# Performance work log

Measured on AMD Instinct MI355X. Metric: run time of the kernel, lower is better.

## Reference

```python
import jax, jax.numpy as jnp
import numpy as np

B, S, H = 2, 4096, 256
NH, NKV = 8, 4
HD = H // NH          # 32
GROUPS = NH // NKV    # 2
ROPE_BASE = 10000.0


def _rope_cos_sin(seq_len, dim, dtype):
    inv_freq = 1.0 / (ROPE_BASE ** (jnp.arange(0, dim, 2, dtype=jnp.float32) / dim))
    t = jnp.arange(seq_len, dtype=jnp.float32)
    freqs = jnp.outer(t, inv_freq)            # [S, dim/2]
    emb = jnp.concatenate([freqs, freqs], -1)  # [S, dim]
    return jnp.cos(emb).astype(dtype), jnp.sin(emb).astype(dtype)


def _rotate_half(x):
    x1, x2 = jnp.split(x, 2, axis=-1)
    return jnp.concatenate([-x2, x1], axis=-1)


def setup_inputs() -> dict:
    key = jax.random.key(0)
    k0, k1, k2, k3, k4 = jax.random.split(key, 5)
    return {
        "hidden_states": jax.random.normal(k0, (B, S, H), jnp.float32),
        "Wq": jax.random.normal(k1, (H, H), jnp.float32) * 0.02,
        "Wk": jax.random.normal(k2, (NKV * HD, H), jnp.float32) * 0.02,
        "Wv": jax.random.normal(k3, (NKV * HD, H), jnp.float32) * 0.02,
        "Wo": jax.random.normal(k4, (H, H), jnp.float32) * 0.02,
    }


def reference(hidden_states, Wq, Wk, Wv, Wo):
    b, s, _ = hidden_states.shape
    # projections (nn.Linear: x @ W.T)
    q = (hidden_states @ Wq.T).reshape(b, s, NH, HD).transpose(0, 2, 1, 3)   # [b,nh,s,hd]
    k = (hidden_states @ Wk.T).reshape(b, s, NKV, HD).transpose(0, 2, 1, 3)  # [b,nkv,s,hd]
    v = (hidden_states @ Wv.T).reshape(b, s, NKV, HD).transpose(0, 2, 1, 3)
    # RoPE
    cos, sin = _rope_cos_sin(s, HD, hidden_states.dtype)  # [s,hd]
    q = q * cos + _rotate_half(q) * sin
    k = k * cos + _rotate_half(k) * sin
    # GQA: repeat kv heads (repeat_interleave over head dim)
    k = jnp.repeat(k, GROUPS, axis=1)  # [b,nh,s,hd]
    v = jnp.repeat(v, GROUPS, axis=1)
    # scores + causal mask
    scores = jnp.einsum('bhqd,bhkd->bhqk', q, k) / jnp.sqrt(jnp.float32(HD)).astype(q.dtype)
    causal = jnp.triu(jnp.full((s, s), -jnp.inf, dtype=scores.dtype), k=1)
    scores = scores + causal
    attn = jax.nn.softmax(scores.astype(jnp.float32), axis=-1).astype(q.dtype)
    out = jnp.einsum('bhqk,bhkd->bhqd', attn, v)          # [b,nh,s,hd]
    out = out.transpose(0, 2, 1, 3).reshape(b, s, NH * HD)
    return out @ Wo.T
```

## Files before the change

kernel.cpp:

```cpp
#include <hip/hip_runtime.h>
#include <hip/hip_bf16.h>
#include <stdint.h>

#define NB 2
#define SEQ 4096
#define HID 256
#define NHEAD 8
#define NKVH 4
#define HDIM 32

typedef __bf16 bf16;
typedef __bf16 bf16x8 __attribute__((ext_vector_type(8)));
typedef float f32x4 __attribute__((ext_vector_type(4)));

static __device__ __forceinline__ uint16_t bfbits(float f) {
    bf16 h = (bf16)f;
    return __builtin_bit_cast(uint16_t, h);
}
static __device__ __forceinline__ uint32_t pack_bf16(float lo, float hi) {
    return (uint32_t)bfbits(lo) | ((uint32_t)bfbits(hi) << 16);
}
static __device__ __forceinline__ float fexp2(float x) {
#if __has_builtin(__builtin_amdgcn_exp2f)
    return __builtin_amdgcn_exp2f(x);
#else
    float r; asm("v_exp_f32 %0, %1" : "=v"(r) : "v"(x)); return r;
#endif
}
static __device__ __forceinline__ void gld_lds16(const void* g, void* l) {
    __builtin_amdgcn_global_load_lds(
        (const __attribute__((address_space(1))) void*)g,
        (__attribute__((address_space(3))) void*)l, 16, 0, 0);
}

__global__ __launch_bounds__(256) void qkv_proj(
    const float* __restrict__ hs, const float* __restrict__ Wq,
    const float* __restrict__ Wk, const float* __restrict__ Wv,
    bf16* __restrict__ qws, bf16* __restrict__ kws, bf16* __restrict__ vtws)
{
    __shared__ bf16 As[64][136];
    __shared__ bf16 Bs[64][136];
    const int t = threadIdx.x;
    const int wid = t >> 6, lane = t & 63;
    const int g = lane >> 4, c = lane & 15;
    const int n0 = blockIdx.x * 64;
    const int m0 = blockIdx.y * 64;

    const float* bsrc; int ro;
    if (n0 < 256)      { bsrc = Wq; ro = n0; }
    else if (n0 < 384) { bsrc = Wk; ro = n0 - 256; }
    else               { bsrc = Wv; ro = n0 - 384; }

    const f32x4 zf = {0.f, 0.f, 0.f, 0.f};
    f32x4 acc[4] = {zf, zf, zf, zf};

    const int c4 = t & 31;
    const int rb = t >> 5;

    for (int ks = 0; ks < 256; ks += 128) {
        __syncthreads();
        #pragma unroll
        for (int i = 0; i < 8; ++i) {
            int row = i * 8 + rb;
            float4 v = *(const float4*)&hs[(size_t)(m0 + row) * HID + ks + c4 * 4];
            ushort4 w; w.x = bfbits(v.x); w.y = bfbits(v.y); w.z = bfbits(v.z); w.w = bfbits(v.w);
            *(ushort4*)&As[row][c4 * 4] = w;
        }
        #pragma unroll
        for (int i = 0; i < 8; ++i) {
            int row = i * 8 + rb;
            float4 v = *(const float4*)&bsrc[(size_t)(ro + row) * HID + ks + c4 * 4];
            ushort4 w; w.x = bfbits(v.x); w.y = bfbits(v.y); w.z = bfbits(v.z); w.w = bfbits(v.w);
            *(ushort4*)&Bs[row][c4 * 4] = w;
        }
        __syncthreads();
        #pragma unroll
        for (int kk = 0; kk < 128; kk += 32) {
            bf16x8 af = *(const bf16x8*)&As[wid * 16 + c][kk + g * 8];
            #pragma unroll
            for (int nt = 0; nt < 4; ++nt) {
                bf16x8 bfr = *(const bf16x8*)&Bs[nt * 16 + c][kk + g * 8];
                acc[nt] = __builtin_amdgcn_mfma_f32_16x16x32_bf16(af, bfr, acc[nt], 0, 0, 0);
            }
        }
    }

    const float qscale = 1.4426950408889634f * 0.17677669529663687f;
    const float invf = exp2f(-0.83048202372184f * (float)c);
    #pragma unroll
    for (int r = 0; r < 4; ++r) {
        int m = m0 + wid * 16 + g * 4 + r;
        int b = m >> 12, s = m & (SEQ - 1);
        float sn, cs;
        sincosf((float)s * invf, &sn, &cs);
        if (n0 < 256) {
            #pragma unroll
            for (int np = 0; np < 4; np += 2) {
                int h = (n0 + np * 16) >> 5;
                float x1 = acc[np][r], x2 = acc[np + 1][r];
                float y1 = (x1 * cs - x2 * sn) * qscale;
                float y2 = (x2 * cs + x1 * sn) * qscale;
                size_t base = ((size_t)(b * NHEAD + h) * SEQ + s) * HDIM;
                qws[base + c] = (bf16)y1;
                qws[base + 16 + c] = (bf16)y2;
            }
        } else if (n0 < 384) {
            #pragma unroll
            for (int np = 0; np < 4; np += 2) {
                int kh = (n0 - 256 + np * 16) >> 5;
                float x1 = acc[np][r], x2 = acc[np + 1][r];
                float y1 = x1 * cs - x2 * sn;
                float y2 = x2 * cs + x1 * sn;
                size_t base = ((size_t)(b * NKVH + kh) * SEQ + s) * HDIM;
                kws[base + c] = (bf16)y1;
                kws[base + 16 + c] = (bf16)y2;
            }
        } else {
            #pragma unroll
            for (int nt = 0; nt < 4; ++nt) {
                int ng = n0 + nt * 16 + c - 384;
                int vh = ng >> 5, d = ng & 31;
                vtws[((size_t)(b * NKVH + vh) * HDIM + d) * SEQ + s] = (bf16)acc[nt][r];
            }
        }
    }
}

__global__ __launch_bounds__(256, 2) void attn_fwd(
    const bf16* __restrict__ qws, const bf16* __restrict__ kws,
    const bf16* __restrict__ vtws, bf16* __restrict__ att)
{
    __shared__ bf16 Kb[2][64 * 32];
    __shared__ bf16 Vb[2][32 * 64];
    __shared__ float tr[4][16 * 33];
    const int t = threadIdx.x;
    const int w = t >> 6, lane = t & 63;
    const int g = lane >> 4, c = lane & 15;
    const int wg = blockIdx.x;
    const int h = wg & 7;
    const int rest = wg >> 3;
    const int b = rest & 1;
    const int T = 31 - (rest >> 1);
    const int kvh = h >> 1;
    const bf16* Kg = kws + (size_t)(b * NKVH + kvh) * SEQ * HDIM;
    const bf16* Vg = vtws + (size_t)(b * NKVH + kvh) * HDIM * SEQ;
    const int nsteps = 2 * T + 2;
    const int q0 = T * 128 + w * 32;
    const int d_w = 2 * T + (w >> 1);

    const bf16* Qb = qws + (size_t)(b * NHEAD + h) * SEQ * HDIM;
    bf16x8 qf0 = *(const bf16x8*)&Qb[(size_t)(q0 + c) * HDIM + g * 8];
    bf16x8 qf1 = *(const bf16x8*)&Qb[(size_t)(q0 + 16 + c) * HDIM + g * 8];

    const int sd = t >> 3, sseg = t & 7;
    const bf16* kg_t = Kg + t * 8;
    const bf16* vg_t = Vg + (size_t)sd * SEQ + (sseg ^ (sd & 7)) * 8;
    char* kl[2] = { (char*)&Kb[0][0] + w * 1024, (char*)&Kb[1][0] + w * 1024 };
    char* vl[2] = { (char*)&Vb[0][0] + w * 1024, (char*)&Vb[1][0] + w * 1024 };

    const int kperm = 8 * (c >> 2) + (c & 3);
    const int kro = kperm * 64 + g * 16;
    const int cx = c & 7;
    const int vro0 = c * 128, vro1 = (16 + c) * 128;

    const f32x4 zf = {0.f, 0.f, 0.f, 0.f};
    union { uint32_t u[4]; bf16x8 v; } onesf;
    onesf.u[0] = onesf.u[1] = onesf.u[2] = onesf.u[3] = 0x3F803F80u;

    f32x4 o00 = zf, o01 = zf, ol0 = zf;
    f32x4 o10 = zf, o11 = zf, ol1 = zf;

    gld_lds16(kg_t, kl[0]);
    gld_lds16(vg_t, vl[0]);
    __syncthreads();

    #pragma unroll 1
    for (int s = 0; s < nsteps; ++s) {
        const int sn = s + 1;
        if (sn < nsteps) {
            gld_lds16(kg_t + sn * 2048, kl[sn & 1]);
            gld_lds16(vg_t + sn * 64, vl[sn & 1]);
        }
        if (s <= d_w) {
            const char* kbuf = (const char*)&Kb[s & 1][0];
            const char* vbuf = (const char*)&Vb[s & 1][0];

            bf16x8 kf0 = *(const bf16x8*)(kbuf + kro);
            bf16x8 kf1 = *(const bf16x8*)(kbuf + kro + 256);
            bf16x8 kf2 = *(const bf16x8*)(kbuf + kro + 2048);
            bf16x8 kf3 = *(const bf16x8*)(kbuf + kro + 2304);
            bf16x8 vf00 = *(const bf16x8*)(vbuf + vro0 + ((g ^ cx) << 4));
            bf16x8 vf01 = *(const bf16x8*)(vbuf + vro1 + ((g ^ cx) << 4));
            bf16x8 vf10 = *(const bf16x8*)(vbuf + vro0 + (((4 + g) ^ cx) << 4));
            bf16x8 vf11 = *(const bf16x8*)(vbuf + vro1 + (((4 + g) ^ cx) << 4));

            const bool diag = (s == d_w);
            const int qbase = (w & 1) * 32 + c;

            {
                f32x4 st0 = __builtin_amdgcn_mfma_f32_16x16x32_bf16(kf0, qf0, zf, 0, 0, 0);
                f32x4 st1 = __builtin_amdgcn_mfma_f32_16x16x32_bf16(kf1, qf0, zf, 0, 0, 0);
                f32x4 st2 = __builtin_amdgcn_mfma_f32_16x16x32_bf16(kf2, qf0, zf, 0, 0, 0);
                f32x4 st3 = __builtin_amdgcn_mfma_f32_16x16x32_bf16(kf3, qf0, zf, 0, 0, 0);
                if (diag) {
                    const int qoff = qbase;
                    #pragma unroll
                    for (int r = 0; r < 4; ++r) {
                        if (8 * g + r > qoff)          st0[r] = -1e30f;
                        if (8 * g + 4 + r > qoff)      st1[r] = -1e30f;
                        if (32 + 8 * g + r > qoff)     st2[r] = -1e30f;
                        if (32 + 8 * g + 4 + r > qoff) st3[r] = -1e30f;
                    }
                }
                float p00 = fexp2(st0[0]), p01 = fexp2(st0[1]), p02 = fexp2(st0[2]), p03 = fexp2(st0[3]);
                float p10 = fexp2(st1[0]), p11 = fexp2(st1[1]), p12 = fexp2(st1[2]), p13 = fexp2(st1[3]);
                float p20 = fexp2(st2[0]), p21 = fexp2(st2[1]), p22 = fexp2(st2[2]), p23 = fexp2(st2[3]);
                float p30 = fexp2(st3[0]), p31 = fexp2(st3[1]), p32 = fexp2(st3[2]), p33 = fexp2(st3[3]);
                union { uint32_t u[4]; bf16x8 v; } pb0, pb1;
                asm("v_cvt_pk_bf16_f32 %0, %1, %2" : "=v"(pb0.u[0]) : "v"(p00), "v"(p01));
                asm("v_cvt_pk_bf16_f32 %0, %1, %2" : "=v"(pb0.u[1]) : "v"(p02), "v"(p03));
                asm("v_cvt_pk_bf16_f32 %0, %1, %2" : "=v"(pb0.u[2]) : "v"(p10), "v"(p11));
                asm("v_cvt_pk_bf16_f32 %0, %1, %2" : "=v"(pb0.u[3]) : "v"(p12), "v"(p13));
                asm("v_cvt_pk_bf16_f32 %0, %1, %2" : "=v"(pb1.u[0]) : "v"(p20), "v"(p21));
                asm("v_cvt_pk_bf16_f32 %0, %1, %2" : "=v"(pb1.u[1]) : "v"(p22), "v"(p23));
                asm("v_cvt_pk_bf16_f32 %0, %1, %2" : "=v"(pb1.u[2]) : "v"(p30), "v"(p31));
                asm("v_cvt_pk_bf16_f32 %0, %1, %2" : "=v"(pb1.u[3]) : "v"(p32), "v"(p33));
                o00 = __builtin_amdgcn_mfma_f32_16x16x32_bf16(vf00, pb0.v, o00, 0, 0, 0);
                o01 = __builtin_amdgcn_mfma_f32_16x16x32_bf16(vf01, pb0.v, o01, 0, 0, 0);
                ol0 = __builtin_amdgcn_mfma_f32_16x16x32_bf16(onesf.v, pb0.v, ol0, 0, 0, 0);
                o00 = __builtin_amdgcn_mfma_f32_16x16x32_bf16(vf10, pb1.v, o00, 0, 0, 0);
                o01 = __builtin_amdgcn_mfma_f32_16x16x32_bf16(vf11, pb1.v, o01, 0, 0, 0);
                ol0 = __builtin_amdgcn_mfma_f32_16x16x32_bf16(onesf.v, pb1.v, ol0, 0, 0, 0);
            }
            {
                f32x4 st0 = __builtin_amdgcn_mfma_f32_16x16x32_bf16(kf0, qf1, zf, 0, 0, 0);
                f32x4 st1 = __builtin_amdgcn_mfma_f32_16x16x32_bf16(kf1, qf1, zf, 0, 0, 0);
                f32x4 st2 = __builtin_amdgcn_mfma_f32_16x16x32_bf16(kf2, qf1, zf, 0, 0, 0);
                f32x4 st3 = __builtin_amdgcn_mfma_f32_16x16x32_bf16(kf3, qf1, zf, 0, 0, 0);
                if (diag) {
                    const int qoff = qbase + 16;
                    #pragma unroll
                    for (int r = 0; r < 4; ++r) {
                        if (8 * g + r > qoff)          st0[r] = -1e30f;
                        if (8 * g + 4 + r > qoff)      st1[r] = -1e30f;
                        if (32 + 8 * g + r > qoff)     st2[r] = -1e30f;
                        if (32 + 8 * g + 4 + r > qoff) st3[r] = -1e30f;
                    }
                }
                float p00 = fexp2(st0[0]), p01 = fexp2(st0[1]), p02 = fexp2(st0[2]), p03 = fexp2(st0[3]);
                float p10 = fexp2(st1[0]), p11 = fexp2(st1[1]), p12 = fexp2(st1[2]), p13 = fexp2(st1[3]);
                float p20 = fexp2(st2[0]), p21 = fexp2(st2[1]), p22 = fexp2(st2[2]), p23 = fexp2(st2[3]);
                float p30 = fexp2(st3[0]), p31 = fexp2(st3[1]), p32 = fexp2(st3[2]), p33 = fexp2(st3[3]);
                union { uint32_t u[4]; bf16x8 v; } pb0, pb1;
                asm("v_cvt_pk_bf16_f32 %0, %1, %2" : "=v"(pb0.u[0]) : "v"(p00), "v"(p01));
                asm("v_cvt_pk_bf16_f32 %0, %1, %2" : "=v"(pb0.u[1]) : "v"(p02), "v"(p03));
                asm("v_cvt_pk_bf16_f32 %0, %1, %2" : "=v"(pb0.u[2]) : "v"(p10), "v"(p11));
                asm("v_cvt_pk_bf16_f32 %0, %1, %2" : "=v"(pb0.u[3]) : "v"(p12), "v"(p13));
                asm("v_cvt_pk_bf16_f32 %0, %1, %2" : "=v"(pb1.u[0]) : "v"(p20), "v"(p21));
                asm("v_cvt_pk_bf16_f32 %0, %1, %2" : "=v"(pb1.u[1]) : "v"(p22), "v"(p23));
                asm("v_cvt_pk_bf16_f32 %0, %1, %2" : "=v"(pb1.u[2]) : "v"(p30), "v"(p31));
                asm("v_cvt_pk_bf16_f32 %0, %1, %2" : "=v"(pb1.u[3]) : "v"(p32), "v"(p33));
                o10 = __builtin_amdgcn_mfma_f32_16x16x32_bf16(vf00, pb0.v, o10, 0, 0, 0);
                o11 = __builtin_amdgcn_mfma_f32_16x16x32_bf16(vf01, pb0.v, o11, 0, 0, 0);
                ol1 = __builtin_amdgcn_mfma_f32_16x16x32_bf16(onesf.v, pb0.v, ol1, 0, 0, 0);
                o10 = __builtin_amdgcn_mfma_f32_16x16x32_bf16(vf10, pb1.v, o10, 0, 0, 0);
                o11 = __builtin_amdgcn_mfma_f32_16x16x32_bf16(vf11, pb1.v, o11, 0, 0, 0);
                ol1 = __builtin_amdgcn_mfma_f32_16x16x32_bf16(onesf.v, pb1.v, ol1, 0, 0, 0);
            }
        }
        __syncthreads();
    }

    #pragma unroll 1
    for (int j = 0; j < 2; ++j) {
        f32x4 a0 = j ? o10 : o00;
        f32x4 a1 = j ? o11 : o01;
        f32x4 al = j ? ol1 : ol0;
        float inv = 1.0f / al[0];
        #pragma unroll
        for (int r = 0; r < 4; ++r) {
            tr[w][c * 33 + 4 * g + r]      = a0[r] * inv;
            tr[w][c * 33 + 16 + 4 * g + r] = a1[r] * inv;
        }
        int q = lane >> 2, dp = (lane & 3) * 8;
        uint32_t u0 = pack_bf16(tr[w][q * 33 + dp + 0], tr[w][q * 33 + dp + 1]);
        uint32_t u1 = pack_bf16(tr[w][q * 33 + dp + 2], tr[w][q * 33 + dp + 3]);
        uint32_t u2 = pack_bf16(tr[w][q * 33 + dp + 4], tr[w][q * 33 + dp + 5]);
        uint32_t u3 = pack_bf16(tr[w][q * 33 + dp + 6], tr[w][q * 33 + dp + 7]);
        size_t base = ((size_t)b * SEQ + q0 + j * 16 + q) * HID + h * HDIM + dp;
        *(uint4*)&att[base] = make_uint4(u0, u1, u2, u3);
    }
}

__global__ __launch_bounds__(256) void out_proj(
    const bf16* __restrict__ att, const float* __restrict__ Wo,
    float* __restrict__ out)
{
    __shared__ bf16 As[64][136];
    __shared__ bf16 Bs[64][136];
    const int t = threadIdx.x;
    const int wid = t >> 6, lane = t & 63;
    const int g = lane >> 4, c = lane & 15;
    const int n0 = blockIdx.x * 64;
    const int m0 = blockIdx.y * 64;

    const f32x4 zf = {0.f, 0.f, 0.f, 0.f};
    f32x4 acc[4] = {zf, zf, zf, zf};

    const int c4 = t & 31;
    const int rb = t >> 5;

    for (int ks = 0; ks < 256; ks += 128) {
        __syncthreads();
        #pragma unroll
        for (int i = 0; i < 8; ++i) {
            int row = i * 8 + rb;
            ushort4 v = *(const ushort4*)&att[(size_t)(m0 + row) * HID + ks + c4 * 4];
            *(ushort4*)&As[row][c4 * 4] = v;
        }
        #pragma unroll
        for (int i = 0; i < 8; ++i) {
            int row = i * 8 + rb;
            float4 v = *(const float4*)&Wo[(size_t)(n0 + row) * HID + ks + c4 * 4];
            ushort4 w; w.x = bfbits(v.x); w.y = bfbits(v.y); w.z = bfbits(v.z); w.w = bfbits(v.w);
            *(ushort4*)&Bs[row][c4 * 4] = w;
        }
        __syncthreads();
        #pragma unroll
        for (int kk = 0; kk < 128; kk += 32) {
            bf16x8 af = *(const bf16x8*)&As[wid * 16 + c][kk + g * 8];
            #pragma unroll
            for (int nt = 0; nt < 4; ++nt) {
                bf16x8 bfr = *(const bf16x8*)&Bs[nt * 16 + c][kk + g * 8];
                acc[nt] = __builtin_amdgcn_mfma_f32_16x16x32_bf16(af, bfr, acc[nt], 0, 0, 0);
            }
        }
    }

    #pragma unroll
    for (int nt = 0; nt < 4; ++nt) {
        #pragma unroll
        for (int r = 0; r < 4; ++r) {
            int m = m0 + wid * 16 + g * 4 + r;
            out[(size_t)m * HID + n0 + nt * 16 + c] = acc[nt][r];
        }
    }
}

extern "C" void kernel_launch(void* const* d_in, const int* in_sizes, int n_in,
                              void* d_out, int out_size, void* d_ws, size_t ws_size,
                              hipStream_t stream) {
    const float* hs = (const float*)d_in[0];
    const float* Wq = (const float*)d_in[1];
    const float* Wk = (const float*)d_in[2];
    const float* Wv = (const float*)d_in[3];
    const float* Wo = (const float*)d_in[4];
    char* ws = (char*)d_ws;
    bf16* qws  = (bf16*)(ws);
    bf16* kws  = (bf16*)(ws + 4194304);
    bf16* vtws = (bf16*)(ws + 6291456);
    bf16* att  = (bf16*)(ws + 8388608);

    qkv_proj<<<dim3(8, 128), 256, 0, stream>>>(hs, Wq, Wk, Wv, qws, kws, vtws);
    attn_fwd<<<512, 256, 0, stream>>>(qws, kws, vtws, att);
    out_proj<<<dim3(4, 128), 256, 0, stream>>>(att, Wo, (float*)d_out);
}
```

Baseline: 68.10 us.

## Triple-buffer K/V loads with vmcnt waits and balance causal tile ordering

Switches the attention K/V LDS staging from double to triple buffering. Two tiles are prefetched ahead, and each step uses an explicit s_waitcnt vmcnt plus a single barrier in place of the two __syncthreads per step. It also changes the block-to-query-tile mapping so that the second half of the grid walks tiles in ascending order, aiming to balance causal work across the two waves of blocks. This costs more LDS per block, which may reduce occupancy, and relies on the hand-placed vmcnt counts being correct.

```diff
diff --git a/kernel.cpp b/kernel.cpp
--- a/kernel.cpp
+++ b/kernel.cpp
@@ -130,17 +130,18 @@
     const bf16* __restrict__ qws, const bf16* __restrict__ kws,
     const bf16* __restrict__ vtws, bf16* __restrict__ att)
 {
-    __shared__ bf16 Kb[2][64 * 32];
-    __shared__ bf16 Vb[2][32 * 64];
+    __shared__ bf16 Kb[3][64 * 32];
+    __shared__ bf16 Vb[3][32 * 64];
     __shared__ float tr[4][16 * 33];
     const int t = threadIdx.x;
     const int w = t >> 6, lane = t & 63;
     const int g = lane >> 4, c = lane & 15;
     const int wg = blockIdx.x;
     const int h = wg & 7;
-    const int rest = wg >> 3;
-    const int b = rest & 1;
-    const int T = 31 - (rest >> 1);
+    const int rem = (wg >> 3) & 31;
+    const int b = rem & 1;
+    const int tp = rem >> 1;
+    const int T = (wg < 256) ? (31 - tp) : tp;
     const int kvh = h >> 1;
     const bf16* Kg = kws + (size_t)(b * NKVH + kvh) * SEQ * HDIM;
     const bf16* Vg = vtws + (size_t)(b * NKVH + kvh) * HDIM * SEQ;
@@ -155,8 +156,8 @@
     const int sd = t >> 3, sseg = t & 7;
     const bf16* kg_t = Kg + t * 8;
     const bf16* vg_t = Vg + (size_t)sd * SEQ + (sseg ^ (sd & 7)) * 8;
-    char* kl[2] = { (char*)&Kb[0][0] + w * 1024, (char*)&Kb[1][0] + w * 1024 };
-    char* vl[2] = { (char*)&Vb[0][0] + w * 1024, (char*)&Vb[1][0] + w * 1024 };
+    char* kls = (char*)&Kb[0][0] + w * 1024;
+    char* vls = (char*)&Vb[0][0] + w * 1024;
 
     const int kperm = 8 * (c >> 2) + (c & 3);
     const int kro = kperm * 64 + g * 16;
@@ -170,20 +171,27 @@
     f32x4 o00 = zf, o01 = zf, ol0 = zf;
     f32x4 o10 = zf, o11 = zf, ol1 = zf;
 
-    gld_lds16(kg_t, kl[0]);
-    gld_lds16(vg_t, vl[0]);
-    __syncthreads();
-
+    gld_lds16(kg_t, kls);
+    gld_lds16(vg_t, vls);
+    gld_lds16(kg_t + 2048, kls + 4096);
+    gld_lds16(vg_t + 64, vls + 4096);
+
+    int rc = 0, ri = 2;
     #pragma unroll 1
     for (int s = 0; s < nsteps; ++s) {
-        const int sn = s + 1;
+        if (s + 1 < nsteps) asm volatile("s_waitcnt vmcnt(2)" ::: "memory");
+        else                asm volatile("s_waitcnt vmcnt(0)" ::: "memory");
+        __builtin_amdgcn_s_barrier();
+        __builtin_amdgcn_sched_barrier(0);
+        const int sn = s + 2;
         if (sn < nsteps) {
-            gld_lds16(kg_t + sn * 2048, kl[sn & 1]);
-            gld_lds16(vg_t + sn * 64, vl[sn & 1]);
-        }
+            gld_lds16(kg_t + (size_t)sn * 2048, kls + ri * 4096);
+            gld_lds16(vg_t + (size_t)sn * 64, vls + ri * 4096);
+        }
+        __builtin_amdgcn_sched_barrier(0);
         if (s <= d_w) {
-            const char* kbuf = (const char*)&Kb[s & 1][0];
-            const char* vbuf = (const char*)&Vb[s & 1][0];
+            const char* kbuf = (const char*)&Kb[0][0] + rc * 4096;
+            const char* vbuf = (const char*)&Vb[0][0] + rc * 4096;
 
             bf16x8 kf0 = *(const bf16x8*)(kbuf + kro);
             bf16x8 kf1 = *(const bf16x8*)(kbuf + kro + 256);
@@ -268,7 +276,8 @@
                 ol1 = __builtin_amdgcn_mfma_f32_16x16x32_bf16(onesf.v, pb1.v, ol1, 0, 0, 0);
             }
         }
-        __syncthreads();
+        rc = (rc == 2) ? 0 : rc + 1;
+        ri = (ri == 2) ? 0 : ri + 1;
     }
 
     #pragma unroll 1
```

After: 83.65 us. +22.8%, slower.

## Use 128-key KV tiles per step with per-wave diagonal skipping and reordered block schedule

Applied to the files above, without the earlier changes.

Each pipeline step now stages 128 keys of K and V into LDS instead of 64, which halves the number of loop iterations and __syncthreads barriers per block. Within a step the work is split into four 32-key chunks, and on the diagonal tile each wave skips the chunks that lie entirely above its causal boundary. The block-to-tile mapping also changes so the second half of the grid runs tiles in ascending order, which pairs heavy and light causal tiles. LDS usage doubles, which may limit occupancy, and the V swizzle and load addressing are reworked.

```diff
diff --git a/kernel.cpp b/kernel.cpp
--- a/kernel.cpp
+++ b/kernel.cpp
@@ -130,38 +130,43 @@
     const bf16* __restrict__ qws, const bf16* __restrict__ kws,
     const bf16* __restrict__ vtws, bf16* __restrict__ att)
 {
-    __shared__ bf16 Kb[2][64 * 32];
-    __shared__ bf16 Vb[2][32 * 64];
+    __shared__ bf16 Kb[2][128 * 32];
+    __shared__ bf16 Vb[2][32 * 128];
     __shared__ float tr[4][16 * 33];
     const int t = threadIdx.x;
     const int w = t >> 6, lane = t & 63;
     const int g = lane >> 4, c = lane & 15;
     const int wg = blockIdx.x;
     const int h = wg & 7;
-    const int rest = wg >> 3;
-    const int b = rest & 1;
-    const int T = 31 - (rest >> 1);
+    const int rem = (wg >> 3) & 31;
+    const int b = rem & 1;
+    const int tp = rem >> 1;
+    const int T = (wg < 256) ? (31 - tp) : tp;
     const int kvh = h >> 1;
     const bf16* Kg = kws + (size_t)(b * NKVH + kvh) * SEQ * HDIM;
     const bf16* Vg = vtws + (size_t)(b * NKVH + kvh) * HDIM * SEQ;
-    const int nsteps = 2 * T + 2;
+    const int nsteps = T + 1;
     const int q0 = T * 128 + w * 32;
-    const int d_w = 2 * T + (w >> 1);
 
     const bf16* Qb = qws + (size_t)(b * NHEAD + h) * SEQ * HDIM;
     bf16x8 qf0 = *(const bf16x8*)&Qb[(size_t)(q0 + c) * HDIM + g * 8];
     bf16x8 qf1 = *(const bf16x8*)&Qb[(size_t)(q0 + 16 + c) * HDIM + g * 8];
 
-    const int sd = t >> 3, sseg = t & 7;
     const bf16* kg_t = Kg + t * 8;
-    const bf16* vg_t = Vg + (size_t)sd * SEQ + (sseg ^ (sd & 7)) * 8;
-    char* kl[2] = { (char*)&Kb[0][0] + w * 1024, (char*)&Kb[1][0] + w * 1024 };
-    char* vl[2] = { (char*)&Vb[0][0] + w * 1024, (char*)&Vb[1][0] + w * 1024 };
+    const int seg_s = (t & 8) | ((t & 7) ^ ((t >> 4) & 7));
+    const bf16* vg_tA = Vg + (size_t)(t >> 4) * SEQ + seg_s * 8;
+    const bf16* vg_tB = vg_tA + (size_t)16 * SEQ;
+    char* kl = (char*)&Kb[0][0] + w * 1024;
+    char* vl = (char*)&Vb[0][0] + w * 1024;
 
     const int kperm = 8 * (c >> 2) + (c & 3);
     const int kro = kperm * 64 + g * 16;
     const int cx = c & 7;
-    const int vro0 = c * 128, vro1 = (16 + c) * 128;
+    const int vrow0 = c * 256;
+    const int voff0 = ((g) ^ cx) << 4;
+    const int voff1 = ((4 + g) ^ cx) << 4;
+    const int voff2 = 128 + voff0;
+    const int voff3 = 128 + voff1;
 
     const f32x4 zf = {0.f, 0.f, 0.f, 0.f};
     union { uint32_t u[4]; bf16x8 v; } onesf;
@@ -170,102 +175,76 @@
     f32x4 o00 = zf, o01 = zf, ol0 = zf;
     f32x4 o10 = zf, o11 = zf, ol1 = zf;
 
-    gld_lds16(kg_t, kl[0]);
-    gld_lds16(vg_t, vl[0]);
+    gld_lds16(kg_t, kl);
+    gld_lds16(kg_t + 2048, kl + 4096);
+    gld_lds16(vg_tA, vl);
+    gld_lds16(vg_tB, vl + 4096);
     __syncthreads();
 
     #pragma unroll 1
     for (int s = 0; s < nsteps; ++s) {
         const int sn = s + 1;
         if (sn < nsteps) {
-            gld_lds16(kg_t + sn * 2048, kl[sn & 1]);
-            gld_lds16(vg_t + sn * 64, vl[sn & 1]);
-        }
-        if (s <= d_w) {
-            const char* kbuf = (const char*)&Kb[s & 1][0];
-            const char* vbuf = (const char*)&Vb[s & 1][0];
-
-            bf16x8 kf0 = *(const bf16x8*)(kbuf + kro);
-            bf16x8 kf1 = *(const bf16x8*)(kbuf + kro + 256);
-            bf16x8 kf2 = *(const bf16x8*)(kbuf + kro + 2048);
-            bf16x8 kf3 = *(const bf16x8*)(kbuf + kro + 2304);
-            bf16x8 vf00 = *(const bf16x8*)(vbuf + vro0 + ((g ^ cx) << 4));
-            bf16x8 vf01 = *(const bf16x8*)(vbuf + vro1 + ((g ^ cx) << 4));
-            bf16x8 vf10 = *(const bf16x8*)(vbuf + vro0 + (((4 + g) ^ cx) << 4));
-            bf16x8 vf11 = *(const bf16x8*)(vbuf + vro1 + (((4 + g) ^ cx) << 4));
-
-            const bool diag = (s == d_w);
-            const int qbase = (w & 1) * 32 + c;
-
+            const int bo = (sn & 1) * 8192;
+            gld_lds16(kg_t + (size_t)sn * 4096, kl + bo);
+            gld_lds16(kg_t + (size_t)sn * 4096 + 2048, kl + bo + 4096);
+            gld_lds16(vg_tA + (size_t)sn * 128, vl + bo);
+            gld_lds16(vg_tB + (size_t)sn * 128, vl + bo + 4096);
+        }
+        const char* kbuf = (const char*)&Kb[s & 1][0];
+        const char* vbuf = (const char*)&Vb[s & 1][0];
+        const bool diag = (s == T);
+        const int qo0 = w * 32 + c;
+        #pragma unroll
+        for (int j = 0; j < 4; ++j) {
+            if (diag && j > w) continue;
+            const int voffj = (j == 0) ? voff0 : (j == 1) ? voff1 : (j == 2) ? voff2 : voff3;
+            bf16x8 kf0 = *(const bf16x8*)(kbuf + j * 2048 + kro);
+            bf16x8 kf1 = *(const bf16x8*)(kbuf + j * 2048 + kro + 256);
+            bf16x8 vfA = *(const bf16x8*)(vbuf + vrow0 + voffj);
+            bf16x8 vfB = *(const bf16x8*)(vbuf + 4096 + vrow0 + voffj);
             {
                 f32x4 st0 = __builtin_amdgcn_mfma_f32_16x16x32_bf16(kf0, qf0, zf, 0, 0, 0);
                 f32x4 st1 = __builtin_amdgcn_mfma_f32_16x16x32_bf16(kf1, qf0, zf, 0, 0, 0);
-                f32x4 st2 = __builtin_amdgcn_mfma_f32_16x16x32_bf16(kf2, qf0, zf, 0, 0, 0);
-                f32x4 st3 = __builtin_amdgcn_mfma_f32_16x16x32_bf16(kf3, qf0, zf, 0, 0, 0);
                 if (diag) {
-                    const int qoff = qbase;
                     #pragma unroll
                     for (int r = 0; r < 4; ++r) {
-                        if (8 * g + r > qoff)          st0[r] = -1e30f;
-                        if (8 * g + 4 + r > qoff)      st1[r] = -1e30f;
-                        if (32 + 8 * g + r > qoff)     st2[r] = -1e30f;
-                        if (32 + 8 * g + 4 + r > qoff) st3[r] = -1e30f;
+                        if (j * 32 + 8 * g + r > qo0)     st0[r] = -1e30f;
+                        if (j * 32 + 8 * g + 4 + r > qo0) st1[r] = -1e30f;
                     }
                 }
-                float p00 = fexp2(st0[0]), p01 = fexp2(st0[1]), p02 = fexp2(st0[2]), p03 = fexp2(st0[3]);
-                float p10 = fexp2(st1[0]), p11 = fexp2(st1[1]), p12 = fexp2(st1[2]), p13 = fexp2(st1[3]);
-                float p20 = fexp2(st2[0]), p21 = fexp2(st2[1]), p22 = fexp2(st2[2]), p23 = fexp2(st2[3]);
-                float p30 = fexp2(st3[0]), p31 = fexp2(st3[1]), p32 = fexp2(st3[2]), p33 = fexp2(st3[3]);
-                union { uint32_t u[4]; bf16x8 v; } pb0, pb1;
-                asm("v_cvt_pk_bf16_f32 %0, %1, %2" : "=v"(pb0.u[0]) : "v"(p00), "v"(p01));
-                asm("v_cvt_pk_bf16_f32 %0, %1, %2" : "=v"(pb0.u[1]) : "v"(p02), "v"(p03));
-                asm("v_cvt_pk_bf16_f32 %0, %1, %2" : "=v"(pb0.u[2]) : "v"(p10), "v"(p11));
-                asm("v_cvt_pk_bf16_f32 %0, %1, %2" : "=v"(pb0.u[3]) : "v"(p12), "v"(p13));
-                asm("v_cvt_pk_bf16_f32 %0, %1, %2" : "=v"(pb1.u[0]) : "v"(p20), "v"(p21));
-                asm("v_cvt_pk_bf16_f32 %0, %1, %2" : "=v"(pb1.u[1]) : "v"(p22), "v"(p23));
-                asm("v_cvt_pk_bf16_f32 %0, %1, %2" : "=v"(pb1.u[2]) : "v"(p30), "v"(p31));
-                asm("v_cvt_pk_bf16_f32 %0, %1, %2" : "=v"(pb1.u[3]) : "v"(p32), "v"(p33));
-                o00 = __builtin_amdgcn_mfma_f32_16x16x32_bf16(vf00, pb0.v, o00, 0, 0, 0);
-                o01 = __builtin_amdgcn_mfma_f32_16x16x32_bf16(vf01, pb0.v, o01, 0, 0, 0);
-                ol0 = __builtin_amdgcn_mfma_f32_16x16x32_bf16(onesf.v, pb0.v, ol0, 0, 0, 0);
-                o00 = __builtin_amdgcn_mfma_f32_16x16x32_bf16(vf10, pb1.v, o00, 0, 0, 0);
-                o01 = __builtin_amdgcn_mfma_f32_16x16x32_bf16(vf11, pb1.v, o01, 0, 0, 0);
-                ol0 = __builtin_amdgcn_mfma_f32_16x16x32_bf16(onesf.v, pb1.v, ol0, 0, 0, 0);
+                float p0 = fexp2(st0[0]), p1 = fexp2(st0[1]), p2 = fexp2(st0[2]), p3 = fexp2(st0[3]);
+                float p4 = fexp2(st1[0]), p5 = fexp2(st1[1]), p6 = fexp2(st1[2]), p7 = fexp2(st1[3]);
+                union { uint32_t u[4]; bf16x8 v; } pb;
+                asm("v_cvt_pk_bf16_f32 %0, %1, %2" : "=v"(pb.u[0]) : "v"(p0), "v"(p1));
+                asm("v_cvt_pk_bf16_f32 %0, %1, %2" : "=v"(pb.u[1]) : "v"(p2), "v"(p3));
+                asm("v_cvt_pk_bf16_f32 %0, %1, %2" : "=v"(pb.u[2]) : "v"(p4), "v"(p5));
+                asm("v_cvt_pk_bf16_f32 %0, %1, %2" : "=v"(pb.u[3]) : "v"(p6), "v"(p7));
+                o00 = __builtin_amdgcn_mfma_f32_16x16x32_bf16(vfA, pb.v, o00, 0, 0, 0);
+                o01 = __builtin_amdgcn_mfma_f32_16x16x32_bf16(vfB, pb.v, o01, 0, 0, 0);
+                ol0 = __builtin_amdgcn_mfma_f32_16x16x32_bf16(onesf.v, pb.v, ol0, 0, 0, 0);
             }
             {
                 f32x4 st0 = __builtin_amdgcn_mfma_f32_16x16x32_bf16(kf0, qf1, zf, 0, 0, 0);
                 f32x4 st1 = __builtin_amdgcn_mfma_f32_16x16x32_bf16(kf1, qf1, zf, 0, 0, 0);
-                f32x4 st2 = __builtin_amdgcn_mfma_f32_16x16x32_bf16(kf2, qf1, zf, 0, 0, 0);
-                f32x4 st3 = __builtin_amdgcn_mfma_f32_16x16x32_bf16(kf3, qf1, zf, 0, 0, 0);
                 if (diag) {
-                    const int qoff = qbase + 16;
+                    const int qo1 = qo0 + 16;
                     #pragma unroll
                     for (int r = 0; r < 4; ++r) {
-                        if (8 * g + r > qoff)          st0[r] = -1e30f;
-                        if (8 * g + 4 + r > qoff)      st1[r] = -1e30f;
-                        if (32 + 8 * g + r > qoff)     st2[r] = -1e30f;
-                        if (32 + 8 * g + 4 + r > qoff) st3[r] = -1e30f;
+                        if (j * 32 + 8 * g + r > qo1)     st0[r] = -1e30f;
+                        if (j * 32 + 8 * g + 4 + r > qo1) st1[r] = -1e30f;
                     }
                 }
-                float p00 = fexp2(st0[0]), p01 = fexp2(st0[1]), p02 = fexp2(st0[2]), p03 = fexp2(st0[3]);
-                float p10 = fexp2(st1[0]), p11 = fexp2(st1[1]), p12 = fexp2(st1[2]), p13 = fexp2(st1[3]);
-                float p20 = fexp2(st2[0]), p21 = fexp2(st2[1]), p22 = fexp2(st2[2]), p23 = fexp2(st2[3]);
-                float p30 = fexp2(st3[0]), p31 = fexp2(st3[1]), p32 = fexp2(st3[2]), p33 = fexp2(st3[3]);
-                union { uint32_t u[4]; bf16x8 v; } pb0, pb1;
-                asm("v_cvt_pk_bf16_f32 %0, %1, %2" : "=v"(pb0.u[0]) : "v"(p00), "v"(p01));
-                asm("v_cvt_pk_bf16_f32 %0, %1, %2" : "=v"(pb0.u[1]) : "v"(p02), "v"(p03));
-                asm("v_cvt_pk_bf16_f32 %0, %1, %2" : "=v"(pb0.u[2]) : "v"(p10), "v"(p11));
-                asm("v_cvt_pk_bf16_f32 %0, %1, %2" : "=v"(pb0.u[3]) : "v"(p12), "v"(p13));
-                asm("v_cvt_pk_bf16_f32 %0, %1, %2" : "=v"(pb1.u[0]) : "v"(p20), "v"(p21));
-                asm("v_cvt_pk_bf16_f32 %0, %1, %2" : "=v"(pb1.u[1]) : "v"(p22), "v"(p23));
-                asm("v_cvt_pk_bf16_f32 %0, %1, %2" : "=v"(pb1.u[2]) : "v"(p30), "v"(p31));
-                asm("v_cvt_pk_bf16_f32 %0, %1, %2" : "=v"(pb1.u[3]) : "v"(p32), "v"(p33));
-                o10 = __builtin_amdgcn_mfma_f32_16x16x32_bf16(vf00, pb0.v, o10, 0, 0, 0);
-                o11 = __builtin_amdgcn_mfma_f32_16x16x32_bf16(vf01, pb0.v, o11, 0, 0, 0);
-                ol1 = __builtin_amdgcn_mfma_f32_16x16x32_bf16(onesf.v, pb0.v, ol1, 0, 0, 0);
-                o10 = __builtin_amdgcn_mfma_f32_16x16x32_bf16(vf10, pb1.v, o10, 0, 0, 0);
-                o11 = __builtin_amdgcn_mfma_f32_16x16x32_bf16(vf11, pb1.v, o11, 0, 0, 0);
-                ol1 = __builtin_amdgcn_mfma_f32_16x16x32_bf16(onesf.v, pb1.v, ol1, 0, 0, 0);
+                float p0 = fexp2(st0[0]), p1 = fexp2(st0[1]), p2 = fexp2(st0[2]), p3 = fexp2(st0[3]);
+                float p4 = fexp2(st1[0]), p5 = fexp2(st1[1]), p6 = fexp2(st1[2]), p7 = fexp2(st1[3]);
+                union { uint32_t u[4]; bf16x8 v; } pb;
+                asm("v_cvt_pk_bf16_f32 %0, %1, %2" : "=v"(pb.u[0]) : "v"(p0), "v"(p1));
+                asm("v_cvt_pk_bf16_f32 %0, %1, %2" : "=v"(pb.u[1]) : "v"(p2), "v"(p3));
+                asm("v_cvt_pk_bf16_f32 %0, %1, %2" : "=v"(pb.u[2]) : "v"(p4), "v"(p5));
+                asm("v_cvt_pk_bf16_f32 %0, %1, %2" : "=v"(pb.u[3]) : "v"(p6), "v"(p7));
+                o10 = __builtin_amdgcn_mfma_f32_16x16x32_bf16(vfA, pb.v, o10, 0, 0, 0);
+                o11 = __builtin_amdgcn_mfma_f32_16x16x32_bf16(vfB, pb.v, o11, 0, 0, 0);
+                ol1 = __builtin_amdgcn_mfma_f32_16x16x32_bf16(onesf.v, pb.v, ol1, 0, 0, 0);
             }
         }
         __syncthreads();
```

New measurement: 72.96 us. 7.1% more time.

## Split attention KV range across two workgroups and merge in out_proj

Applied to the files above, without the earlier changes.

Each query tile's causal key range is split into two halves handled by separate workgroups, doubling the grid to 1024 blocks. Unnormalized fp32 partial outputs and row sums are written to workspace, and out_proj sums the halves and normalizes them while loading its A tile. The goal is more parallelism and better load balance across CUs. The cost is extra fp32 global traffic and more work in out_proj. The path is enabled only when the workspace is large enough.

```diff
diff --git a/kernel.cpp b/kernel.cpp
--- a/kernel.cpp
+++ b/kernel.cpp
@@ -126,9 +126,12 @@
     }
 }
 
+template<int SPLIT>
 __global__ __launch_bounds__(256, 2) void attn_fwd(
     const bf16* __restrict__ qws, const bf16* __restrict__ kws,
-    const bf16* __restrict__ vtws, bf16* __restrict__ att)
+    const bf16* __restrict__ vtws, bf16* __restrict__ att,
+    float* __restrict__ Oa, float* __restrict__ Ob,
+    float* __restrict__ la, float* __restrict__ lb)
 {
     __shared__ bf16 Kb[2][64 * 32];
     __shared__ bf16 Vb[2][32 * 64];
@@ -138,13 +141,24 @@
     const int g = lane >> 4, c = lane & 15;
     const int wg = blockIdx.x;
     const int h = wg & 7;
-    const int rest = wg >> 3;
-    const int b = rest & 1;
-    const int T = 31 - (rest >> 1);
+    int T, b, half;
+    if (SPLIT) {
+        const int rest = wg >> 3;
+        half = rest & 1;
+        const int r2 = rest >> 1;
+        b = r2 & 1;
+        T = 31 - (r2 >> 1);
+    } else {
+        const int rest = wg >> 3;
+        half = 0;
+        b = rest & 1;
+        T = 31 - (rest >> 1);
+    }
     const int kvh = h >> 1;
     const bf16* Kg = kws + (size_t)(b * NKVH + kvh) * SEQ * HDIM;
     const bf16* Vg = vtws + (size_t)(b * NKVH + kvh) * HDIM * SEQ;
-    const int nsteps = 2 * T + 2;
+    const int cbase = SPLIT ? half * (T + 1) : 0;
+    const int nloc = SPLIT ? (T + 1) : (2 * T + 2);
     const int q0 = T * 128 + w * 32;
     const int d_w = 2 * T + (w >> 1);
 
@@ -170,18 +184,19 @@
     f32x4 o00 = zf, o01 = zf, ol0 = zf;
     f32x4 o10 = zf, o11 = zf, ol1 = zf;
 
-    gld_lds16(kg_t, kl[0]);
-    gld_lds16(vg_t, vl[0]);
+    gld_lds16(kg_t + (size_t)cbase * 2048, kl[0]);
+    gld_lds16(vg_t + (size_t)cbase * 64, vl[0]);
     __syncthreads();
 
     #pragma unroll 1
-    for (int s = 0; s < nsteps; ++s) {
+    for (int s = 0; s < nloc; ++s) {
+        const int ci = cbase + s;
         const int sn = s + 1;
-        if (sn < nsteps) {
-            gld_lds16(kg_t + sn * 2048, kl[sn & 1]);
-            gld_lds16(vg_t + sn * 64, vl[sn & 1]);
-        }
-        if (s <= d_w) {
+        if (sn < nloc) {
+            gld_lds16(kg_t + (size_t)(cbase + sn) * 2048, kl[sn & 1]);
+            gld_lds16(vg_t + (size_t)(cbase + sn) * 64, vl[sn & 1]);
+        }
+        if (ci <= d_w) {
             const char* kbuf = (const char*)&Kb[s & 1][0];
             const char* vbuf = (const char*)&Vb[s & 1][0];
 
@@ -194,7 +209,7 @@
             bf16x8 vf10 = *(const bf16x8*)(vbuf + vro0 + (((4 + g) ^ cx) << 4));
             bf16x8 vf11 = *(const bf16x8*)(vbuf + vro1 + (((4 + g) ^ cx) << 4));
 
-            const bool diag = (s == d_w);
+            const bool diag = (ci == d_w);
             const int qbase = (w & 1) * 32 + c;
 
             {
@@ -276,25 +291,47 @@
         f32x4 a0 = j ? o10 : o00;
         f32x4 a1 = j ? o11 : o01;
         f32x4 al = j ? ol1 : ol0;
-        float inv = 1.0f / al[0];
-        #pragma unroll
-        for (int r = 0; r < 4; ++r) {
-            tr[w][c * 33 + 4 * g + r]      = a0[r] * inv;
-            tr[w][c * 33 + 16 + 4 * g + r] = a1[r] * inv;
-        }
-        int q = lane >> 2, dp = (lane & 3) * 8;
-        uint32_t u0 = pack_bf16(tr[w][q * 33 + dp + 0], tr[w][q * 33 + dp + 1]);
-        uint32_t u1 = pack_bf16(tr[w][q * 33 + dp + 2], tr[w][q * 33 + dp + 3]);
-        uint32_t u2 = pack_bf16(tr[w][q * 33 + dp + 4], tr[w][q * 33 + dp + 5]);
-        uint32_t u3 = pack_bf16(tr[w][q * 33 + dp + 6], tr[w][q * 33 + dp + 7]);
-        size_t base = ((size_t)b * SEQ + q0 + j * 16 + q) * HID + h * HDIM + dp;
-        *(uint4*)&att[base] = make_uint4(u0, u1, u2, u3);
-    }
-}
-
+        if (SPLIT) {
+            #pragma unroll
+            for (int r = 0; r < 4; ++r) {
+                tr[w][c * 33 + 4 * g + r]      = a0[r];
+                tr[w][c * 33 + 16 + 4 * g + r] = a1[r];
+            }
+            float* Op = half ? Ob : Oa;
+            float* lp = half ? lb : la;
+            if (g == 0) lp[((size_t)b * SEQ + q0 + j * 16 + c) * 8 + h] = al[0];
+            int q = lane >> 2, dp = (lane & 3) * 8;
+            size_t m = (size_t)b * SEQ + q0 + j * 16 + q;
+            float4 f0 = make_float4(tr[w][q * 33 + dp + 0], tr[w][q * 33 + dp + 1],
+                                    tr[w][q * 33 + dp + 2], tr[w][q * 33 + dp + 3]);
+            float4 f1 = make_float4(tr[w][q * 33 + dp + 4], tr[w][q * 33 + dp + 5],
+                                    tr[w][q * 33 + dp + 6], tr[w][q * 33 + dp + 7]);
+            *(float4*)&Op[m * HID + h * HDIM + dp]     = f0;
+            *(float4*)&Op[m * HID + h * HDIM + dp + 4] = f1;
+        } else {
+            float inv = 1.0f / al[0];
+            #pragma unroll
+            for (int r = 0; r < 4; ++r) {
+                tr[w][c * 33 + 4 * g + r]      = a0[r] * inv;
+                tr[w][c * 33 + 16 + 4 * g + r] = a1[r] * inv;
+            }
+            int q = lane >> 2, dp = (lane & 3) * 8;
+            uint32_t u0 = pack_bf16(tr[w][q * 33 + dp + 0], tr[w][q * 33 + dp + 1]);
+            uint32_t u1 = pack_bf16(tr[w][q * 33 + dp + 2], tr[w][q * 33 + dp + 3]);
+            uint32_t u2 = pack_bf16(tr[w][q * 33 + dp + 4], tr[w][q * 33 + dp + 5]);
+            uint32_t u3 = pack_bf16(tr[w][q * 33 + dp + 6], tr[w][q * 33 + dp + 7]);
+            size_t base = ((size_t)b * SEQ + q0 + j * 16 + q) * HID + h * HDIM + dp;
+            *(uint4*)&att[base] = make_uint4(u0, u1, u2, u3);
+        }
+    }
+}
+
+template<int SPLIT>
 __global__ __launch_bounds__(256) void out_proj(
-    const bf16* __restrict__ att, const float* __restrict__ Wo,
-    float* __restrict__ out)
+    const bf16* __restrict__ att,
+    const float* __restrict__ Oa, const float* __restrict__ Ob,
+    const float* __restrict__ la, const float* __restrict__ lb,
+    const float* __restrict__ Wo, float* __restrict__ out)
 {
     __shared__ bf16 As[64][136];
     __shared__ bf16 Bs[64][136];
@@ -315,8 +352,23 @@
         #pragma unroll
         for (int i = 0; i < 8; ++i) {
             int row = i * 8 + rb;
-            ushort4 v = *(const ushort4*)&att[(size_t)(m0 + row) * HID + ks + c4 * 4];
-            *(ushort4*)&As[row][c4 * 4] = v;
+            if (SPLIT) {
+                const size_t m = (size_t)(m0 + row);
+                const int n = ks + c4 * 4;
+                float4 xa = *(const float4*)&Oa[m * HID + n];
+                float4 xb = *(const float4*)&Ob[m * HID + n];
+                const int hh = n >> 5;
+                float inv = 1.0f / (la[m * 8 + hh] + lb[m * 8 + hh]);
+                ushort4 w;
+                w.x = bfbits((xa.x + xb.x) * inv);
+                w.y = bfbits((xa.y + xb.y) * inv);
+                w.z = bfbits((xa.z + xb.z) * inv);
+                w.w = bfbits((xa.w + xb.w) * inv);
+                *(ushort4*)&As[row][c4 * 4] = w;
+            } else {
+                ushort4 v = *(const ushort4*)&att[(size_t)(m0 + row) * HID + ks + c4 * 4];
+                *(ushort4*)&As[row][c4 * 4] = v;
+            }
         }
         #pragma unroll
         for (int i = 0; i < 8; ++i) {
@@ -360,8 +412,18 @@
     bf16* kws  = (bf16*)(ws + 4194304);
     bf16* vtws = (bf16*)(ws + 6291456);
     bf16* att  = (bf16*)(ws + 8388608);
+    float* Oa  = (float*)(ws + 8388608);
+    float* Ob  = (float*)(ws + 16777216);
+    float* la  = (float*)(ws + 25165824);
+    float* lb  = (float*)(ws + 25427968);
+    const bool split = (ws_size >= 25690112);
 
     qkv_proj<<<dim3(8, 128), 256, 0, stream>>>(hs, Wq, Wk, Wv, qws, kws, vtws);
-    attn_fwd<<<512, 256, 0, stream>>>(qws, kws, vtws, att);
-    out_proj<<<dim3(4, 128), 256, 0, stream>>>(att, Wo, (float*)d_out);
-}
+    if (split) {
+        attn_fwd<1><<<1024, 256, 0, stream>>>(qws, kws, vtws, att, Oa, Ob, la, lb);
+        out_proj<1><<<dim3(4, 128), 256, 0, stream>>>(att, Oa, Ob, la, lb, Wo, (float*)d_out);
+    } else {
+        attn_fwd<0><<<512, 256, 0, stream>>>(qws, kws, vtws, att, Oa, Ob, la, lb);
+        out_proj<0><<<dim3(4, 128), 256, 0, stream>>>(att, Oa, Ob, la, lb, Wo, (float*)d_out);
+    }
+}
```

New measurement: 69.79 us. 2.5% more time.
